# Kernel optimization log

Hardware: AMD Instinct MI355X
Metric: run time of the kernel (lower is better)

## Reference

```python
import jax, jax.numpy as jnp
from jax import lax
import numpy as np

NEG_SLOPE = 0.01  # nn.LeakyReLU default


def conv1d(x, w, b, stride=1, padding=0, groups=1):
    # x: (N, C, L), w: (O, C//groups, K), torch Conv1d semantics
    y = lax.conv_general_dilated(
        x, w, window_strides=(stride,), padding=[(padding, padding)],
        dimension_numbers=('NCH', 'OIH', 'NCH'), feature_group_count=groups)
    return y + b[None, :, None]


def maxpool1d_ceil(x, k, s):
    # torch max_pool1d with ceil_mode=True: window may overhang right edge
    L = x.shape[-1]
    out_len = -(-(L - k) // s) + 1  # ceil((L-k)/s)+1
    pad = max(0, (out_len - 1) * s + k - L)
    xp = jnp.pad(x, ((0, 0), (0, 0), (0, pad)), constant_values=-jnp.inf)
    return lax.reduce_window(xp, -jnp.inf, lax.max, (1, 1, k), (1, 1, s), 'VALID')


def adaptive_maxpool1d(x, out_size):
    # Spatial_LSTM_block.get_adaptive_pool (ceil_mode=False default)
    L = x.shape[-1]
    s = L // out_size
    k = L - (out_size - 1) * s
    return lax.reduce_window(x, -jnp.inf, lax.max, (1, 1, k), (1, 1, s), 'VALID')


def lstm_last_h(xseq, w_ih, b_ih, w_hh, b_hh):
    # xseq: (T, B, F); PyTorch LSTMCell gate order: i, f, g, o
    B = xseq.shape[1]
    H = w_hh.shape[1]
    h0 = jnp.zeros((B, H), dtype=xseq.dtype)
    c0 = jnp.zeros((B, H), dtype=xseq.dtype)

    def step(carry, xt):
        h, c = carry
        g = xt @ w_ih.T + b_ih + h @ w_hh.T + b_hh  # (B, 4H)
        i, f, gg, o = jnp.split(g, 4, axis=-1)
        c = jax.nn.sigmoid(f) * c + jax.nn.sigmoid(i) * jnp.tanh(gg)
        h = jax.nn.sigmoid(o) * jnp.tanh(c)
        return (h, c), None

    (h, _), _ = lax.scan(step, (h0, c0), xseq)
    return h


def setup_inputs() -> dict:
    ks = jax.random.split(jax.random.key(0), 32)
    def rn(i, shape, s=0.05):
        return jax.random.normal(ks[i], shape, dtype=jnp.float32) * s
    return {
        'X': jax.random.normal(ks[0], (64, 16, 4096), dtype=jnp.float32),
        # depthwise conv: 16 -> 16*16=256, k=30, groups=16
        'w_dw': rn(1, (256, 1, 30)), 'b_dw': rn(2, (256,)),
        # pointwise conv: 256 -> 32, k=1
        'w_pw': rn(3, (32, 256, 1)), 'b_pw': rn(4, (32,)),
        # conv2: 32 -> 64, k=10
        'w_c2': rn(5, (64, 32, 10)), 'b_c2': rn(6, (64,)),
        # pyramid branch 0 (bin=300): conv 64->4 k=3 p=1, LSTMCell(4,64), Linear(64,1)
        'w_sc0': rn(7, (4, 64, 3)), 'b_sc0': rn(8, (4,)),
        'w_ih0': rn(9, (256, 4)), 'b_ih0': rn(10, (256,)),
        'w_hh0': rn(11, (256, 64)), 'b_hh0': rn(12, (256,)),
        'w_lin0': rn(13, (1, 64)), 'b_lin0': rn(14, (1,)),
        # pyramid branch 1 (bin=100)
        'w_sc1': rn(15, (4, 64, 3)), 'b_sc1': rn(16, (4,)),
        'w_ih1': rn(17, (256, 4)), 'b_ih1': rn(18, (256,)),
        'w_hh1': rn(19, (256, 64)), 'b_hh1': rn(20, (256,)),
        'w_lin1': rn(21, (1, 64)), 'b_lin1': rn(22, (1,)),
        # final head: Linear(len(bins)=2 -> 1), sigmoid
        'w_rul': rn(23, (1, 2)), 'b_rul': rn(24, (1,)),
    }


def reference(X, w_dw, b_dw, w_pw, b_pw, w_c2, b_c2,
              w_sc0, b_sc0, w_ih0, b_ih0, w_hh0, b_hh0, w_lin0, b_lin0,
              w_sc1, b_sc1, w_ih1, b_ih1, w_hh1, b_hh1, w_lin1, b_lin1,
              w_rul, b_rul):
    PYRAMID_BINS = (300, 100)
    x = conv1d(X, w_dw, b_dw, groups=16)            # (B, 256, 4067)
    x = conv1d(x, w_pw, b_pw)                        # (B, 32, 4067)
    x = jax.nn.leaky_relu(x, NEG_SLOPE)
    x = maxpool1d_ceil(x, 20, 5)                     # (B, 32, 811)
    x = conv1d(x, w_c2, b_c2)                        # (B, 64, 802)
    x = jax.nn.leaky_relu(x, NEG_SLOPE)
    branches = [
        (w_sc0, b_sc0, w_ih0, b_ih0, w_hh0, b_hh0, w_lin0, b_lin0),
        (w_sc1, b_sc1, w_ih1, b_ih1, w_hh1, b_hh1, w_lin1, b_lin1),
    ]
    outs = []
    for bin_size, (wsc, bsc, wih, bih, whh, bhh, wl, bl) in zip(PYRAMID_BINS, branches):
        xp = adaptive_maxpool1d(x, bin_size)          # (B, 64, bin)
        xc = jax.nn.leaky_relu(conv1d(xp, wsc, bsc, padding=1), NEG_SLOPE)  # (B, 4, bin)
        seq = jnp.transpose(xc, (2, 0, 1))            # (T, B, 4)
        h = lstm_last_h(seq, wih, bih, whh, bhh)      # (B, 64)
        outs.append(h @ wl.T + bl)                    # (B, 1)
    y = jnp.concatenate(outs, axis=1)                 # (B, 2)
    return jax.nn.sigmoid(y @ w_rul.T + b_rul)        # (B, 1)
```

## Files before the change

kernel.cpp:

```cpp
#include <hip/hip_runtime.h>
#include <cstddef>


typedef __attribute__((ext_vector_type(8))) short bf16x8;
typedef __attribute__((ext_vector_type(4))) float f32x4;
typedef unsigned int uint32;

#define LOG2E 1.4426950408889634f

__device__ __forceinline__ unsigned short f2bf(float f) {
    unsigned u = __float_as_uint(f);
    u += 0x7fffu + ((u >> 16) & 1u);
    return (unsigned short)(u >> 16);
}
__device__ __forceinline__ float bf2f(unsigned short h) {
    return __uint_as_float(((unsigned)h) << 16);
}
__device__ __forceinline__ float exp2_(float x) {
#if __has_builtin(__builtin_amdgcn_exp2f)
    return __builtin_amdgcn_exp2f(x);
#else
    return __expf(0.6931471805599453f * x);
#endif
}
__device__ __forceinline__ float rcp2(float x) {
    return __builtin_amdgcn_rcpf(1.0f + exp2_(x));
}
__device__ __forceinline__ float sigm(float x) {
    return __builtin_amdgcn_rcpf(1.0f + __expf(-x));
}
__device__ __forceinline__ float leaky(float v) { return v >= 0.0f ? v : 0.01f * v; }

__global__ void prep_kernel(const float* __restrict__ w_dw, const float* __restrict__ b_dw,
                            const float* __restrict__ w_pw, const float* __restrict__ b_pw,
                            unsigned short* __restrict__ Wp1, float* __restrict__ b_eff) {
    const int bid = blockIdx.x, tid = threadIdx.x;
    if (bid < 15) {
        const int kc = bid;
        for (int it = 0; it < 4; ++it) {
            int idx = tid + it * 256;
            int n = idx >> 5, kp = idx & 31;
            int ch = kp & 15, kappa = kc * 2 + (kp >> 4);
            float s = 0.f;
            for (int j = 0; j < 16; ++j)
                s += w_pw[n * 256 + ch * 16 + j] * w_dw[(ch * 16 + j) * 30 + kappa];
            Wp1[(kc * 32 + n) * 32 + kp] = f2bf(s);
        }
    } else if (tid < 32) {
        float s = b_pw[tid];
        for (int c = 0; c < 256; ++c) s += w_pw[tid * 256 + c] * b_dw[c];
        b_eff[tid] = s;
    }
}

__global__ __launch_bounds__(256) void conv1p_kernel(const float* __restrict__ X,
        const unsigned short* __restrict__ Wp1, const float* __restrict__ b_eff,
        unsigned short* __restrict__ S2b, int* __restrict__ cnt) {
    const int b = blockIdx.y, tx = blockIdx.x, tid = threadIdx.x;
    if (tx == 0 && b == 0 && tid == 0) *cnt = 0;
    const int l0 = tx * 160;
    __shared__ __align__(16) unsigned short Wl[480 * 40];
    __shared__ __align__(16) unsigned short U[192 * 33];
    unsigned short* Xt = U;
    {
        const int4* s4 = (const int4*)Wp1;
        for (int j = tid; j < 1920; j += 256)
            *(int4*)((uint32*)Wl + (j >> 2) * 20 + (j & 3) * 4) = s4[j];
    }
    for (int i = tid; i < 896; i += 256) {
        int ch = i / 56, p4 = (i - ch * 56) * 4;
        int l = l0 + p4;
        float4 v = {0.f, 0.f, 0.f, 0.f};
        const float* xrow = X + ((size_t)b * 16 + ch) * 4096;
        if (l + 3 < 4096 && p4 + 3 < 221) {
            v = *(const float4*)(xrow + l);
        } else {
            float* vv = (float*)&v;
#pragma unroll
            for (int e = 0; e < 4; ++e) {
                int p = p4 + e, le = l + e;
                vv[e] = (p < 221 && le < 4096) ? xrow[le] : 0.f;
            }
        }
        unsigned short* dst = Xt + p4 * 24 + ch;
        dst[0] = f2bf(v.x); dst[24] = f2bf(v.y); dst[48] = f2bf(v.z); dst[72] = f2bf(v.w);
    }
    __syncthreads();
    const int w = tid >> 6, lane = tid & 63, quad = lane >> 4, l16 = lane & 15;
    const int ki = quad >> 1, ch0 = (quad & 1) * 8;
    f32x4 acc[3][2];
#pragma unroll
    for (int mi = 0; mi < 3; ++mi)
#pragma unroll
        for (int nt = 0; nt < 2; ++nt) acc[mi][nt] = (f32x4){0.f, 0.f, 0.f, 0.f};
#pragma unroll
    for (int kc = 0; kc < 15; ++kc) {
        bf16x8 B0 = *(const bf16x8*)(Wl + (kc * 32 + l16) * 40 + quad * 8);
        bf16x8 B1 = *(const bf16x8*)(Wl + (kc * 32 + 16 + l16) * 40 + quad * 8);
#pragma unroll
        for (int mi = 0; mi < 3; ++mi) {
            int mrow = (w + mi * 4) * 16 + l16 + 2 * kc + ki;
            bf16x8 A = *(const bf16x8*)(Xt + mrow * 24 + ch0);
            acc[mi][0] = __builtin_amdgcn_mfma_f32_16x16x32_bf16(A, B0, acc[mi][0], 0, 0, 0);
            acc[mi][1] = __builtin_amdgcn_mfma_f32_16x16x32_bf16(A, B1, acc[mi][1], 0, 0, 0);
        }
    }
    __syncthreads();
    unsigned short* Ct = U;
#pragma unroll
    for (int mi = 0; mi < 3; ++mi) {
        int lrow = (w + mi * 4) * 16 + quad * 4;
#pragma unroll
        for (int nt = 0; nt < 2; ++nt) {
            int o = nt * 16 + l16;
            float be = b_eff[o];
#pragma unroll
            for (int r = 0; r < 4; ++r)
                Ct[(lrow + r) * 33 + o] = f2bf(leaky(acc[mi][nt][r] + be));
        }
    }
    __syncthreads();
    for (int idx = tid; idx < 1024; idx += 256) {
        int ti = idx >> 5, ch = idx & 31;
        int t = tx * 32 + ti;
        if (t < 811) {
            int pmax = 4067 - 5 * t; if (pmax > 20) pmax = 20;
            int pbase = 5 * ti;
            float m = bf2f(Ct[pbase * 33 + ch]);
            for (int p = 1; p < pmax; ++p) m = fmaxf(m, bf2f(Ct[(pbase + p) * 33 + ch]));
            S2b[((size_t)b * 32 + ch) * 812 + t] = f2bf(m);
        }
    }
}

__global__ __launch_bounds__(256) void conv2_kernel(const unsigned short* __restrict__ S2b,
        const float* __restrict__ w_c2, const float* __restrict__ b_c2,
        float* __restrict__ S3) {
    const int b = blockIdx.y, l0 = blockIdx.x * 64, tid = threadIdx.x;
    __shared__ __align__(16) unsigned short At[80 * 40];
    __shared__ __align__(16) unsigned short Wl[10 * 64 * 40];
    for (int pair = tid; pair < 2048; pair += 256) {
        int n = pair >> 5, kp = pair & 31;
        const float* src = w_c2 + n * 320 + kp * 10;
        unsigned short* dstc = Wl + n * 40 + kp;
#pragma unroll
        for (int kc = 0; kc < 10; ++kc) dstc[kc * 2560] = f2bf(src[kc]);
    }
    for (int i = tid; i < 2560; i += 256) {
        int ch = i / 80, p = i - ch * 80;
        int l = l0 + p;
        At[p * 40 + ch] = (p < 73 && l < 811)
            ? S2b[((size_t)b * 32 + ch) * 812 + l] : (unsigned short)0;
    }
    __syncthreads();
    const int w = tid >> 6, lane = tid & 63, quad = lane >> 4, l16 = lane & 15;
    const int mA = w * 16 + l16, ch0 = quad * 8;
    f32x4 acc[4];
#pragma unroll
    for (int nt = 0; nt < 4; ++nt) acc[nt] = (f32x4){0.f, 0.f, 0.f, 0.f};
#pragma unroll
    for (int kc = 0; kc < 10; ++kc) {
        bf16x8 A = *(const bf16x8*)(At + (mA + kc) * 40 + ch0);
#pragma unroll
        for (int nt = 0; nt < 4; ++nt) {
            bf16x8 Bf = *(const bf16x8*)(Wl + (kc * 64 + nt * 16 + l16) * 40 + quad * 8);
            acc[nt] = __builtin_amdgcn_mfma_f32_16x16x32_bf16(A, Bf, acc[nt], 0, 0, 0);
        }
    }
    const int lbase = l0 + w * 16 + quad * 4;
#pragma unroll
    for (int nt = 0; nt < 4; ++nt) {
        int o = nt * 16 + l16;
        float bc = b_c2[o];
#pragma unroll
        for (int r = 0; r < 4; ++r) {
            int l = lbase + r;
            if (l < 802) S3[((size_t)b * 64 + o) * 802 + l] = leaky(acc[nt][r] + bc);
        }
    }
}

__global__ __launch_bounds__(1024) void branch_kernel(const float* __restrict__ S3,
        const float* __restrict__ w_sc0, const float* __restrict__ b_sc0,
        const float* __restrict__ w_ih0, const float* __restrict__ b_ih0, const float* __restrict__ b_hh0,
        const float* __restrict__ w_sc1, const float* __restrict__ b_sc1,
        const float* __restrict__ w_ih1, const float* __restrict__ b_ih1, const float* __restrict__ b_hh1,
        float* __restrict__ Xg0, float* __restrict__ Xg1) {
    const int b = blockIdx.x, br = blockIdx.y;
    const int T = br ? 100 : 300;
    const float* w_sc = br ? w_sc1 : w_sc0;
    const float* b_sc = br ? b_sc1 : b_sc0;
    const float* w_ih = br ? w_ih1 : w_ih0;
    const float* b_ih = br ? b_ih1 : b_ih0;
    const float* b_hh = br ? b_hh1 : b_hh0;
    float* Xg = br ? Xg1 : Xg0;

    __shared__ float bufs[16][2][402];
    __shared__ unsigned short Ps[64][302];
    __shared__ float xcs[4][304];
    const int tid = threadIdx.x, wv = tid >> 6, lane = tid & 63;

    for (int ci = 0; ci < 4; ++ci) {
        const int c = wv * 4 + ci;
        const float* row = S3 + ((size_t)b * 64 + c) * 802;
        if (br == 0) {
            float* A = bufs[wv][0];
            float* B = bufs[wv][1];
            for (int it = 0; it < 7; ++it) {
                int q = lane + it * 64;
                if (q < 401) A[q] = fmaxf(row[2 * q], row[2 * q + 1]);
            }
            int len = 401;
#pragma unroll
            for (int sp = 1; sp <= 32; sp <<= 1) {
                int nl = len - sp;
                for (int it = 0; it < 7; ++it) {
                    int q = lane + it * 64;
                    if (q < nl) B[q] = fmaxf(A[q], A[q + sp]);
                }
                float* tmp = A; A = B; B = tmp; len = nl;
            }
            for (int it = 0; it < 5; ++it) {
                int t = lane + it * 64;
                if (t < 300) Ps[c][1 + t] = f2bf(fmaxf(A[t], A[t + 38]));
            }
            if (lane < 2) Ps[c][lane * 301] = 0;
        } else {
            for (int it = 0; it < 2; ++it) {
                int t = lane + it * 64;
                if (t < 100) {
                    float m = row[8 * t];
#pragma unroll
                    for (int p = 1; p < 10; ++p) m = fmaxf(m, row[8 * t + p]);
                    Ps[c][1 + t] = f2bf(m);
                }
            }
            if (lane < 2) Ps[c][lane * 101] = 0;
        }
    }
    __syncthreads();
    for (int i = tid; i < 4 * T; i += 1024) {
        int o = i / T, t = i - o * T;
        float sum = b_sc[o];
        const float* wvp = w_sc + o * 192;
        for (int c = 0; c < 64; ++c) {
            float p0 = bf2f(Ps[c][t]), p1 = bf2f(Ps[c][t + 1]), p2 = bf2f(Ps[c][t + 2]);
            sum += wvp[c * 3] * p0 + wvp[c * 3 + 1] * p1 + wvp[c * 3 + 2] * p2;
        }
        xcs[o][t] = leaky(sum);
    }
    __syncthreads();
    {
        const int h = tid & 63, tq = tid >> 6;
        const int wv2 = h >> 4, l16 = h & 15;
        const int bt = b >> 2, q = b & 3;
        const float4 w0 = *(const float4*)(w_ih + (0 * 64 + h) * 4);
        const float4 w1 = *(const float4*)(w_ih + (1 * 64 + h) * 4);
        const float4 w2 = *(const float4*)(w_ih + (2 * 64 + h) * 4);
        const float4 w3 = *(const float4*)(w_ih + (3 * 64 + h) * 4);
        const float b0 = b_ih[0 * 64 + h] + b_hh[0 * 64 + h];
        const float b1 = b_ih[1 * 64 + h] + b_hh[1 * 64 + h];
        const float b2 = b_ih[2 * 64 + h] + b_hh[2 * 64 + h];
        const float b3 = b_ih[3 * 64 + h] + b_hh[3 * 64 + h];
        const float scA = -LOG2E, scG = -2.0f * LOG2E;
        float4* Xg4 = (float4*)Xg;
        const size_t slot = ((size_t)(bt * 4 + wv2) * 4 + q) * 16 + l16;
        for (int t = tq; t < T; t += 16) {
            float x0 = xcs[0][t], x1 = xcs[1][t], x2 = xcs[2][t], x3 = xcs[3][t];
            float v0 = b0 + w0.x * x0 + w0.y * x1 + w0.z * x2 + w0.w * x3;
            float v1 = b1 + w1.x * x0 + w1.y * x1 + w1.z * x2 + w1.w * x3;
            float v2 = b2 + w2.x * x0 + w2.y * x1 + w2.z * x2 + w2.w * x3;
            float v3 = b3 + w3.x * x0 + w3.y * x1 + w3.z * x2 + w3.w * x3;
            float4 ov = {scA * v0, scA * v1, scG * v2, scA * v3};
            Xg4[(size_t)t * 4096 + slot] = ov;
        }
    }
}

#define HPAD 72
__global__ __launch_bounds__(256) void lstm_kernel(
    const float* __restrict__ Xg0, const float* __restrict__ Xg1,
    const float* __restrict__ Whh0, const float* __restrict__ Whh1,
    const float* __restrict__ wl0, const float* __restrict__ bl0,
    const float* __restrict__ wl1, const float* __restrict__ bl1,
    float* __restrict__ brbuf, int* __restrict__ cnt,
    const float* __restrict__ w_rul, const float* __restrict__ b_rul,
    float* __restrict__ out) {
    const int bt = blockIdx.x;
    const int br = blockIdx.y;
    const int T = (br == 0) ? 300 : 100;
    const float* Xg = (br == 0) ? Xg0 : Xg1;
    const float* Whh = (br == 0) ? Whh0 : Whh1;
    const float* wl = (br == 0) ? wl0 : wl1;
    const float* bl = (br == 0) ? bl0 : bl1;
    const float C2L = -2.0f * LOG2E;

    __shared__ __align__(16) unsigned short h_lds[2][16][HPAD];
    __shared__ int lastf;

    const int tid = threadIdx.x;
    const int w = tid >> 6, lane = tid & 63, quad = lane >> 4, l16 = lane & 15;
    const int hidx = w * 16 + l16;

    bf16x8 Bf[4][2];
#pragma unroll
    for (int g = 0; g < 4; ++g) {
        const int n = g * 64 + hidx;
        const float scg = (g == 2) ? (-2.0f * LOG2E) : (-LOG2E);
#pragma unroll
        for (int kc = 0; kc < 2; ++kc) {
            const float* src = Whh + n * 64 + kc * 32 + quad * 8;
            bf16x8 v;
#pragma unroll
            for (int j = 0; j < 8; ++j) v[j] = (short)f2bf(src[j] * scg);
            Bf[g][kc] = v;
        }
    }

    for (int i = tid; i < 2 * 16 * HPAD; i += 256) (&h_lds[0][0][0])[i] = 0;

    const float* xp = Xg + (((size_t)bt * 4 + w) * 4 + quad) * 64 + l16 * 4;

    f32x4 xq[4];
#pragma unroll
    for (int j = 0; j < 4; ++j) xq[j] = *(const f32x4*)(xp + (size_t)j * 16384);

    float c0 = 0.f;

    __syncthreads();

    auto step = [&](int t, f32x4& xb) {
        const unsigned short* hrow = &h_lds[t & 1][l16][0];
        bf16x8 A0 = *(const bf16x8*)(hrow + quad * 8);
        bf16x8 A1 = *(const bf16x8*)(hrow + 32 + quad * 8);
        const f32x4 z = {0.f, 0.f, 0.f, 0.f};
        f32x4 ac[4];
#pragma unroll
        for (int g = 0; g < 4; ++g) {
            ac[g] = __builtin_amdgcn_mfma_f32_16x16x32_bf16(A0, Bf[g][0], z, 0, 0, 0);
            ac[g] = __builtin_amdgcn_mfma_f32_16x16x32_bf16(A1, Bf[g][1], ac[g], 0, 0, 0);
        }
        float iv = rcp2(ac[0][0] + xb[0]);
        float fv = rcp2(ac[1][0] + xb[1]);
        float gv = 2.0f * rcp2(ac[2][0] + xb[2]) - 1.0f;
        float ov = rcp2(ac[3][0] + xb[3]);
        if (t + 4 < T) xb = *(const f32x4*)(xp + (size_t)(t + 4) * 16384);
        float cs = fv * c0 + iv * gv;
        c0 = cs;
        float rr = __builtin_amdgcn_rcpf(1.0f + exp2_(cs * C2L));
        float hv = fmaf(2.0f * ov, rr, -ov);
        h_lds[(t + 1) & 1][quad * 4][hidx] = f2bf(hv);
        asm volatile("s_waitcnt lgkmcnt(0)\n\ts_barrier" ::: "memory");
    };

    for (int t = 0; t < T; t += 4) {
#pragma unroll
        for (int j = 0; j < 4; ++j) step(t + j, xq[j]);
    }

    __syncthreads();

    if (tid < 4) {
        const unsigned short* hrow = &h_lds[0][tid * 4][0];
        float s = bl[0];
        for (int j = 0; j < 64; ++j) s += bf2f(hrow[j]) * wl[j];
        atomicExch(&brbuf[br * 64 + bt * 4 + tid], s);
    }
    __syncthreads();
    __threadfence();
    if (tid == 0) {
        int old = atomicAdd(cnt, 1);
        lastf = (old == 31);
    }
    __syncthreads();
    if (lastf) {
        __threadfence();
        if (tid < 64) {
            float v0 = atomicAdd(&brbuf[tid], 0.0f);
            float v1 = atomicAdd(&brbuf[64 + tid], 0.0f);
            float v = w_rul[0] * v0 + w_rul[1] * v1 + b_rul[0];
            out[tid] = sigm(v);
        }
    }
}

extern "C" void kernel_launch(void* const* d_in, const int* in_sizes, int n_in,
                              void* d_out, int out_size, void* d_ws, size_t ws_size,
                              hipStream_t stream) {
    const float* X     = (const float*)d_in[0];
    const float* w_dw  = (const float*)d_in[1];
    const float* b_dw  = (const float*)d_in[2];
    const float* w_pw  = (const float*)d_in[3];
    const float* b_pw  = (const float*)d_in[4];
    const float* w_c2  = (const float*)d_in[5];
    const float* b_c2  = (const float*)d_in[6];
    const float* w_sc0 = (const float*)d_in[7];
    const float* b_sc0 = (const float*)d_in[8];
    const float* w_ih0 = (const float*)d_in[9];
    const float* b_ih0 = (const float*)d_in[10];
    const float* w_hh0 = (const float*)d_in[11];
    const float* b_hh0 = (const float*)d_in[12];
    const float* w_l0  = (const float*)d_in[13];
    const float* b_l0  = (const float*)d_in[14];
    const float* w_sc1 = (const float*)d_in[15];
    const float* b_sc1 = (const float*)d_in[16];
    const float* w_ih1 = (const float*)d_in[17];
    const float* b_ih1 = (const float*)d_in[18];
    const float* w_hh1 = (const float*)d_in[19];
    const float* b_hh1 = (const float*)d_in[20];
    const float* w_l1  = (const float*)d_in[21];
    const float* b_l1  = (const float*)d_in[22];
    const float* w_rul = (const float*)d_in[23];
    const float* b_rul = (const float*)d_in[24];

    float* ws = (float*)d_ws;
    float* Xg0 = ws;
    float* Xg1 = ws + 4915200;
    unsigned short* S2b = (unsigned short*)(ws + 6553600);
    float* S3    = ws + 7385088;
    unsigned short* Wp1 = (unsigned short*)(ws + 10670080);
    float* b_eff = ws + 10677760;
    float* brbuf = ws + 10677792;
    int*   cnt   = (int*)(ws + 10677920);

    prep_kernel<<<16, 256, 0, stream>>>(w_dw, b_dw, w_pw, b_pw, Wp1, b_eff);
    conv1p_kernel<<<dim3(26, 64), 256, 0, stream>>>(X, Wp1, b_eff, S2b, cnt);
    conv2_kernel<<<dim3(13, 64), 256, 0, stream>>>(S2b, w_c2, b_c2, S3);
    branch_kernel<<<dim3(64, 2), 1024, 0, stream>>>(
        S3, w_sc0, b_sc0, w_ih0, b_ih0, b_hh0,
            w_sc1, b_sc1, w_ih1, b_ih1, b_hh1, Xg0, Xg1);
    lstm_kernel<<<dim3(16, 2), 256, 0, stream>>>(Xg0, Xg1, w_hh0, w_hh1,
                                                 w_l0, b_l0, w_l1, b_l1,
                                                 brbuf, cnt, w_rul, b_rul, (float*)d_out);
}
```

Before: 325.2 us.

## Fuse conv2 and pyramid branch preprocessing into one per-batch kernel

Merges the conv2 MFMA kernel and the branch kernel into a single 1024-thread block per batch element. The conv2 tiles and the branch scratch share LDS through a union, and both pyramid branches are handled serially in the same block. This removes one kernel launch and its launch gap, and the S3 rows are read back by the same block (likely from cache). In exchange, parallelism drops from 832+128 blocks to 64 blocks, and the branches no longer run concurrently.

```diff
diff --git a/kernel.cpp b/kernel.cpp
--- a/kernel.cpp
+++ b/kernel.cpp
@@ -133,146 +133,161 @@
     }
 }
 
-__global__ __launch_bounds__(256) void conv2_kernel(const unsigned short* __restrict__ S2b,
+__global__ __launch_bounds__(1024) void c2br_kernel(const unsigned short* __restrict__ S2b,
         const float* __restrict__ w_c2, const float* __restrict__ b_c2,
-        float* __restrict__ S3) {
-    const int b = blockIdx.y, l0 = blockIdx.x * 64, tid = threadIdx.x;
-    __shared__ __align__(16) unsigned short At[80 * 40];
-    __shared__ __align__(16) unsigned short Wl[10 * 64 * 40];
-    for (int pair = tid; pair < 2048; pair += 256) {
-        int n = pair >> 5, kp = pair & 31;
-        const float* src = w_c2 + n * 320 + kp * 10;
-        unsigned short* dstc = Wl + n * 40 + kp;
-#pragma unroll
-        for (int kc = 0; kc < 10; ++kc) dstc[kc * 2560] = f2bf(src[kc]);
-    }
-    for (int i = tid; i < 2560; i += 256) {
-        int ch = i / 80, p = i - ch * 80;
-        int l = l0 + p;
-        At[p * 40 + ch] = (p < 73 && l < 811)
-            ? S2b[((size_t)b * 32 + ch) * 812 + l] : (unsigned short)0;
-    }
-    __syncthreads();
-    const int w = tid >> 6, lane = tid & 63, quad = lane >> 4, l16 = lane & 15;
-    const int mA = w * 16 + l16, ch0 = quad * 8;
-    f32x4 acc[4];
-#pragma unroll
-    for (int nt = 0; nt < 4; ++nt) acc[nt] = (f32x4){0.f, 0.f, 0.f, 0.f};
-#pragma unroll
-    for (int kc = 0; kc < 10; ++kc) {
-        bf16x8 A = *(const bf16x8*)(At + (mA + kc) * 40 + ch0);
-#pragma unroll
-        for (int nt = 0; nt < 4; ++nt) {
-            bf16x8 Bf = *(const bf16x8*)(Wl + (kc * 64 + nt * 16 + l16) * 40 + quad * 8);
-            acc[nt] = __builtin_amdgcn_mfma_f32_16x16x32_bf16(A, Bf, acc[nt], 0, 0, 0);
-        }
-    }
-    const int lbase = l0 + w * 16 + quad * 4;
-#pragma unroll
-    for (int nt = 0; nt < 4; ++nt) {
-        int o = nt * 16 + l16;
-        float bc = b_c2[o];
-#pragma unroll
-        for (int r = 0; r < 4; ++r) {
-            int l = lbase + r;
-            if (l < 802) S3[((size_t)b * 64 + o) * 802 + l] = leaky(acc[nt][r] + bc);
-        }
-    }
-}
-
-__global__ __launch_bounds__(1024) void branch_kernel(const float* __restrict__ S3,
+        float* __restrict__ S3,
         const float* __restrict__ w_sc0, const float* __restrict__ b_sc0,
         const float* __restrict__ w_ih0, const float* __restrict__ b_ih0, const float* __restrict__ b_hh0,
         const float* __restrict__ w_sc1, const float* __restrict__ b_sc1,
         const float* __restrict__ w_ih1, const float* __restrict__ b_ih1, const float* __restrict__ b_hh1,
         float* __restrict__ Xg0, float* __restrict__ Xg1) {
-    const int b = blockIdx.x, br = blockIdx.y;
-    const int T = br ? 100 : 300;
-    const float* w_sc = br ? w_sc1 : w_sc0;
-    const float* b_sc = br ? b_sc1 : b_sc0;
-    const float* w_ih = br ? w_ih1 : w_ih0;
-    const float* b_ih = br ? b_ih1 : b_ih0;
-    const float* b_hh = br ? b_hh1 : b_hh0;
-    float* Xg = br ? Xg1 : Xg0;
-
-    __shared__ float bufs[16][2][402];
-    __shared__ unsigned short Ps[64][302];
-    __shared__ float xcs[4][304];
-    const int tid = threadIdx.x, wv = tid >> 6, lane = tid & 63;
-
-    for (int ci = 0; ci < 4; ++ci) {
-        const int c = wv * 4 + ci;
-        const float* row = S3 + ((size_t)b * 64 + c) * 802;
-        if (br == 0) {
-            float* A = bufs[wv][0];
-            float* B = bufs[wv][1];
-            for (int it = 0; it < 7; ++it) {
-                int q = lane + it * 64;
-                if (q < 401) A[q] = fmaxf(row[2 * q], row[2 * q + 1]);
-            }
-            int len = 401;
-#pragma unroll
-            for (int sp = 1; sp <= 32; sp <<= 1) {
-                int nl = len - sp;
+    const int b = blockIdx.x, tid = threadIdx.x;
+
+    __shared__ __align__(16) union SmemU {
+        struct { unsigned short Wl[10 * 64 * 40]; unsigned short At[4][80 * 40]; } c2;
+        struct { float bufs[16][2][402]; unsigned short Ps[64][302]; float xcs[4][304]; } br;
+    } U;
+
+    {
+        const int g = tid >> 8, t256 = tid & 255;
+        for (int pair = tid; pair < 2048; pair += 1024) {
+            int n = pair >> 5, kp = pair & 31;
+            const float* src = w_c2 + n * 320 + kp * 10;
+            unsigned short* dstc = U.c2.Wl + n * 40 + kp;
+#pragma unroll
+            for (int kc = 0; kc < 10; ++kc) dstc[kc * 2560] = f2bf(src[kc]);
+        }
+        for (int r = 0; r < 4; ++r) {
+            const int lt = r * 4 + g;
+            const int l0 = lt * 64;
+            if (lt < 13) {
+                unsigned short* At = U.c2.At[g];
+                for (int i = t256; i < 2560; i += 256) {
+                    int ch = i / 80, p = i - ch * 80;
+                    int l = l0 + p;
+                    At[p * 40 + ch] = (p < 73 && l < 811)
+                        ? S2b[((size_t)b * 32 + ch) * 812 + l] : (unsigned short)0;
+                }
+            }
+            __syncthreads();
+            if (lt < 13) {
+                const unsigned short* At = U.c2.At[g];
+                const int w = t256 >> 6, lane = t256 & 63, quad = lane >> 4, l16 = lane & 15;
+                const int mA = w * 16 + l16, ch0 = quad * 8;
+                f32x4 acc[4];
+#pragma unroll
+                for (int nt = 0; nt < 4; ++nt) acc[nt] = (f32x4){0.f, 0.f, 0.f, 0.f};
+#pragma unroll
+                for (int kc = 0; kc < 10; ++kc) {
+                    bf16x8 A = *(const bf16x8*)(At + (mA + kc) * 40 + ch0);
+#pragma unroll
+                    for (int nt = 0; nt < 4; ++nt) {
+                        bf16x8 Bf = *(const bf16x8*)(U.c2.Wl + (kc * 64 + nt * 16 + l16) * 40 + quad * 8);
+                        acc[nt] = __builtin_amdgcn_mfma_f32_16x16x32_bf16(A, Bf, acc[nt], 0, 0, 0);
+                    }
+                }
+                const int lbase = l0 + w * 16 + quad * 4;
+#pragma unroll
+                for (int nt = 0; nt < 4; ++nt) {
+                    int o = nt * 16 + l16;
+                    float bc = b_c2[o];
+#pragma unroll
+                    for (int r2 = 0; r2 < 4; ++r2) {
+                        int l = lbase + r2;
+                        if (l < 802) S3[((size_t)b * 64 + o) * 802 + l] = leaky(acc[nt][r2] + bc);
+                    }
+                }
+            }
+            __syncthreads();
+        }
+    }
+
+    const int wv = tid >> 6, lane = tid & 63;
+    for (int brv = 0; brv < 2; ++brv) {
+        __syncthreads();
+        const int T = brv ? 100 : 300;
+        const float* w_sc = brv ? w_sc1 : w_sc0;
+        const float* b_sc = brv ? b_sc1 : b_sc0;
+        const float* w_ih = brv ? w_ih1 : w_ih0;
+        const float* b_ih = brv ? b_ih1 : b_ih0;
+        const float* b_hh = brv ? b_hh1 : b_hh0;
+        float* Xg = brv ? Xg1 : Xg0;
+
+        for (int ci = 0; ci < 4; ++ci) {
+            const int c = wv * 4 + ci;
+            const float* row = S3 + ((size_t)b * 64 + c) * 802;
+            if (brv == 0) {
+                float* A = U.br.bufs[wv][0];
+                float* B = U.br.bufs[wv][1];
                 for (int it = 0; it < 7; ++it) {
                     int q = lane + it * 64;
-                    if (q < nl) B[q] = fmaxf(A[q], A[q + sp]);
-                }
-                float* tmp = A; A = B; B = tmp; len = nl;
-            }
-            for (int it = 0; it < 5; ++it) {
-                int t = lane + it * 64;
-                if (t < 300) Ps[c][1 + t] = f2bf(fmaxf(A[t], A[t + 38]));
-            }
-            if (lane < 2) Ps[c][lane * 301] = 0;
-        } else {
-            for (int it = 0; it < 2; ++it) {
-                int t = lane + it * 64;
-                if (t < 100) {
-                    float m = row[8 * t];
-#pragma unroll
-                    for (int p = 1; p < 10; ++p) m = fmaxf(m, row[8 * t + p]);
-                    Ps[c][1 + t] = f2bf(m);
-                }
-            }
-            if (lane < 2) Ps[c][lane * 101] = 0;
-        }
-    }
-    __syncthreads();
-    for (int i = tid; i < 4 * T; i += 1024) {
-        int o = i / T, t = i - o * T;
-        float sum = b_sc[o];
-        const float* wvp = w_sc + o * 192;
-        for (int c = 0; c < 64; ++c) {
-            float p0 = bf2f(Ps[c][t]), p1 = bf2f(Ps[c][t + 1]), p2 = bf2f(Ps[c][t + 2]);
-            sum += wvp[c * 3] * p0 + wvp[c * 3 + 1] * p1 + wvp[c * 3 + 2] * p2;
-        }
-        xcs[o][t] = leaky(sum);
-    }
-    __syncthreads();
-    {
-        const int h = tid & 63, tq = tid >> 6;
-        const int wv2 = h >> 4, l16 = h & 15;
-        const int bt = b >> 2, q = b & 3;
-        const float4 w0 = *(const float4*)(w_ih + (0 * 64 + h) * 4);
-        const float4 w1 = *(const float4*)(w_ih + (1 * 64 + h) * 4);
-        const float4 w2 = *(const float4*)(w_ih + (2 * 64 + h) * 4);
-        const float4 w3 = *(const float4*)(w_ih + (3 * 64 + h) * 4);
-        const float b0 = b_ih[0 * 64 + h] + b_hh[0 * 64 + h];
-        const float b1 = b_ih[1 * 64 + h] + b_hh[1 * 64 + h];
-        const float b2 = b_ih[2 * 64 + h] + b_hh[2 * 64 + h];
-        const float b3 = b_ih[3 * 64 + h] + b_hh[3 * 64 + h];
-        const float scA = -LOG2E, scG = -2.0f * LOG2E;
-        float4* Xg4 = (float4*)Xg;
-        const size_t slot = ((size_t)(bt * 4 + wv2) * 4 + q) * 16 + l16;
-        for (int t = tq; t < T; t += 16) {
-            float x0 = xcs[0][t], x1 = xcs[1][t], x2 = xcs[2][t], x3 = xcs[3][t];
-            float v0 = b0 + w0.x * x0 + w0.y * x1 + w0.z * x2 + w0.w * x3;
-            float v1 = b1 + w1.x * x0 + w1.y * x1 + w1.z * x2 + w1.w * x3;
-            float v2 = b2 + w2.x * x0 + w2.y * x1 + w2.z * x2 + w2.w * x3;
-            float v3 = b3 + w3.x * x0 + w3.y * x1 + w3.z * x2 + w3.w * x3;
-            float4 ov = {scA * v0, scA * v1, scG * v2, scA * v3};
-            Xg4[(size_t)t * 4096 + slot] = ov;
+                    if (q < 401) A[q] = fmaxf(row[2 * q], row[2 * q + 1]);
+                }
+                int len = 401;
+#pragma unroll
+                for (int sp = 1; sp <= 32; sp <<= 1) {
+                    int nl = len - sp;
+                    for (int it = 0; it < 7; ++it) {
+                        int q = lane + it * 64;
+                        if (q < nl) B[q] = fmaxf(A[q], A[q + sp]);
+                    }
+                    float* tmp = A; A = B; B = tmp; len = nl;
+                }
+                for (int it = 0; it < 5; ++it) {
+                    int t = lane + it * 64;
+                    if (t < 300) U.br.Ps[c][1 + t] = f2bf(fmaxf(A[t], A[t + 38]));
+                }
+                if (lane < 2) U.br.Ps[c][lane * 301] = 0;
+            } else {
+                for (int it = 0; it < 2; ++it) {
+                    int t = lane + it * 64;
+                    if (t < 100) {
+                        float m = row[8 * t];
+#pragma unroll
+                        for (int p = 1; p < 10; ++p) m = fmaxf(m, row[8 * t + p]);
+                        U.br.Ps[c][1 + t] = f2bf(m);
+                    }
+                }
+                if (lane < 2) U.br.Ps[c][lane * 101] = 0;
+            }
+        }
+        __syncthreads();
+        for (int i = tid; i < 4 * T; i += 1024) {
+            int o = i / T, t = i - o * T;
+            float sum = b_sc[o];
+            const float* wvp = w_sc + o * 192;
+            for (int c = 0; c < 64; ++c) {
+                float p0 = bf2f(U.br.Ps[c][t]), p1 = bf2f(U.br.Ps[c][t + 1]), p2 = bf2f(U.br.Ps[c][t + 2]);
+                sum += wvp[c * 3] * p0 + wvp[c * 3 + 1] * p1 + wvp[c * 3 + 2] * p2;
+            }
+            U.br.xcs[o][t] = leaky(sum);
+        }
+        __syncthreads();
+        {
+            const int h = tid & 63, tq = tid >> 6;
+            const int wv2 = h >> 4, l16 = h & 15;
+            const int bt = b >> 2, q = b & 3;
+            const float4 w0 = *(const float4*)(w_ih + (0 * 64 + h) * 4);
+            const float4 w1 = *(const float4*)(w_ih + (1 * 64 + h) * 4);
+            const float4 w2 = *(const float4*)(w_ih + (2 * 64 + h) * 4);
+            const float4 w3 = *(const float4*)(w_ih + (3 * 64 + h) * 4);
+            const float b0 = b_ih[0 * 64 + h] + b_hh[0 * 64 + h];
+            const float b1 = b_ih[1 * 64 + h] + b_hh[1 * 64 + h];
+            const float b2 = b_ih[2 * 64 + h] + b_hh[2 * 64 + h];
+            const float b3 = b_ih[3 * 64 + h] + b_hh[3 * 64 + h];
+            const float scA = -LOG2E, scG = -2.0f * LOG2E;
+            float4* Xg4 = (float4*)Xg;
+            const size_t slot = ((size_t)(bt * 4 + wv2) * 4 + q) * 16 + l16;
+            for (int t = tq; t < T; t += 16) {
+                float x0 = U.br.xcs[0][t], x1 = U.br.xcs[1][t];
+                float x2 = U.br.xcs[2][t], x3 = U.br.xcs[3][t];
+                float v0 = b0 + w0.x * x0 + w0.y * x1 + w0.z * x2 + w0.w * x3;
+                float v1 = b1 + w1.x * x0 + w1.y * x1 + w1.z * x2 + w1.w * x3;
+                float v2 = b2 + w2.x * x0 + w2.y * x1 + w2.z * x2 + w2.w * x3;
+                float v3 = b3 + w3.x * x0 + w3.y * x1 + w3.z * x2 + w3.w * x3;
+                float4 ov = {scA * v0, scA * v1, scG * v2, scA * v3};
+                Xg4[(size_t)t * 4096 + slot] = ov;
+            }
         }
     }
 }
@@ -425,10 +440,9 @@
 
     prep_kernel<<<16, 256, 0, stream>>>(w_dw, b_dw, w_pw, b_pw, Wp1, b_eff);
     conv1p_kernel<<<dim3(26, 64), 256, 0, stream>>>(X, Wp1, b_eff, S2b, cnt);
-    conv2_kernel<<<dim3(13, 64), 256, 0, stream>>>(S2b, w_c2, b_c2, S3);
-    branch_kernel<<<dim3(64, 2), 1024, 0, stream>>>(
-        S3, w_sc0, b_sc0, w_ih0, b_ih0, b_hh0,
-            w_sc1, b_sc1, w_ih1, b_ih1, b_hh1, Xg0, Xg1);
+    c2br_kernel<<<64, 1024, 0, stream>>>(S2b, w_c2, b_c2, S3,
+        w_sc0, b_sc0, w_ih0, b_ih0, b_hh0,
+        w_sc1, b_sc1, w_ih1, b_ih1, b_hh1, Xg0, Xg1);
     lstm_kernel<<<dim3(16, 2), 256, 0, stream>>>(Xg0, Xg1, w_hh0, w_hh1,
                                                  w_l0, b_l0, w_l1, b_l1,
                                                  brbuf, cnt, w_rul, b_rul, (float*)d_out);
```

Measured after the change: 347.5 us. 6.8% more time.
